# Kernel optimization log

Hardware: AMD Instinct MI355X
Metric: run time of the kernel (lower is better)

## Reference

```python
import jax, jax.numpy as jnp
from jax import lax
import numpy as np

EPS = 1e-5
GROUPS = 32  # conv_dim // 4 = 128 // 4


def setup_inputs() -> dict:
    key = jax.random.key(0)
    ks = jax.random.split(key, 6)
    B, C, H, W = 32, 256, 64, 64
    S = 64            # state_dim
    CD = 2 * S        # conv_dim = 128
    x = jax.random.normal(ks[0], (B, C, H, W), dtype=jnp.float32)
    ln_w = jnp.ones((1, C, 1, 1), dtype=jnp.float32)
    ln_b = jnp.zeros((1, C, 1, 1), dtype=jnp.float32)
    # conv weights, OIHW, fan-in scaled
    w_bcdt = jax.random.normal(ks[1], (CD, C, 1, 1), dtype=jnp.float32) / np.sqrt(C)
    w_gw = jax.random.normal(ks[2], (CD, CD // GROUPS, 3, 3), dtype=jnp.float32) / np.sqrt(9 * CD // GROUPS)
    w_out = jax.random.normal(ks[3], (C, C, 1, 1), dtype=jnp.float32) / np.sqrt(C)
    # A ~ Uniform(1, 16) per original init range
    A = jax.random.uniform(ks[4], (S,), dtype=jnp.float32, minval=1.0, maxval=16.0)
    return {"x": x, "ln_w": ln_w, "ln_b": ln_b, "w_bcdt": w_bcdt, "w_gw": w_gw, "w_out": w_out, "A": A}


def reference(x, ln_w, ln_b, w_bcdt, w_gw, w_out, A):
    B, C, H, W = x.shape
    N = H * W
    # LayerNorm2D over channel dim; torch.var default is unbiased (correction=1)
    mean = jnp.mean(x, axis=1, keepdims=True)
    var = jnp.sum((x - mean) ** 2, axis=1, keepdims=True) / (C - 1)
    xn = (x - mean) / jnp.sqrt(var + EPS) * ln_w + ln_b
    # BCdt_proj: 1x1 conv (no bias, no norm, no act)
    bcdt = jnp.einsum('bchw,oc->bohw', xn, w_bcdt[:, :, 0, 0])
    # gw: 3x3 grouped conv, padding 1
    bcdt = lax.conv_general_dilated(
        bcdt, w_gw, window_strides=(1, 1), padding=[(1, 1), (1, 1)],
        dimension_numbers=('NCHW', 'OIHW', 'NCHW'), feature_group_count=GROUPS)
    # SSD core
    flat = bcdt.reshape(B, -1, N)                       # (B, 2S, N)
    BC, dt = jnp.split(flat, 2, axis=1)                 # each (B, S, N)
    Asm = jax.nn.softmax(dt + A[None, :, None], axis=-1)
    AB = Asm * BC                                       # (B, S, N)
    xf = x.reshape(B, C, N)
    h = jnp.einsum('bcn,bsn->bcs', xf, AB)              # (B, C, S)
    y = jnp.einsum('bcs,bsn->bcn', h, BC)               # (B, C, N)
    y = y.reshape(B, C, H, W)
    # out_proj: 1x1 conv
    y = jnp.einsum('bchw,oc->bohw', y, w_out[:, :, 0, 0])
    return y + x
```

## Files before the change

kernel.cpp:

```cpp
#include <hip/hip_runtime.h>
#include <math.h>

#define BB 32
#define CC 256
#define NPIX 4096
#define SS 64
#define CD 128

typedef __attribute__((ext_vector_type(8))) short bf16x8;
typedef __attribute__((ext_vector_type(4))) float f32x4;
typedef __attribute__((ext_vector_type(8))) unsigned short us8;

#define WS_W1     0u
#define WS_S1     16384u
#define WS_BIAS   16512u
#define WS_WOUTT  16640u
#define WS_BCDT1  82176u
#define WS_AB     82176u
#define WS_BCT    4276480u
#define WS_HPART  8470784u
#define WS_H2OS   10567936u
#define WS_BCDT2  16859392u

__device__ inline short f2bf(float f) {
    union { float f; unsigned u; } v; v.f = f;
    unsigned r = v.u + 0x7fffu + ((v.u >> 16) & 1u);
    return (short)(r >> 16);
}
__device__ inline float bf2f(unsigned short h) {
    union { unsigned u; float f; } v; v.u = ((unsigned)h) << 16;
    return v.f;
}
__device__ inline bf16x8 cvt8(float4 a, float4 b) {
    bf16x8 r;
    r[0]=f2bf(a.x); r[1]=f2bf(a.y); r[2]=f2bf(a.z); r[3]=f2bf(a.w);
    r[4]=f2bf(b.x); r[5]=f2bf(b.y); r[6]=f2bf(b.z); r[7]=f2bf(b.w);
    return r;
}

__global__ __launch_bounds__(256) void k_setup1(const float* __restrict__ w_bcdt,
        const float* __restrict__ ln_w, const float* __restrict__ ln_b,
        unsigned short* __restrict__ W1, float* __restrict__ S1, float* __restrict__ bias) {
    int o = blockIdx.x, c = threadIdx.x;
    float w = w_bcdt[o*256 + c];
    short h = f2bf(w * ln_w[c]);
    W1[o*256 + c] = (unsigned short)h;
    __shared__ float red[256];
    red[c] = bf2f((unsigned short)h);
    __syncthreads();
    for (int off = 128; off > 0; off >>= 1) { if (c < off) red[c] += red[c+off]; __syncthreads(); }
    if (c == 0) S1[o] = red[0];
    __syncthreads();
    red[c] = w * ln_b[c];
    __syncthreads();
    for (int off = 128; off > 0; off >>= 1) { if (c < off) red[c] += red[c+off]; __syncthreads(); }
    if (c == 0) bias[o] = red[0];
}

__global__ __launch_bounds__(256) void k_setup2(const float* __restrict__ w_out,
        float* __restrict__ w_outT) {
    int o = blockIdx.x, c = threadIdx.x;
    w_outT[c*256 + o] = w_out[o*256 + c];
}

__global__ __launch_bounds__(256) void k_proj(const float* __restrict__ x,
        const unsigned short* __restrict__ W1, const float* __restrict__ S1,
        const float* __restrict__ bias, float* __restrict__ bcdt1) {
    int nbase = blockIdx.x * 64;
    int b = blockIdx.y;
    int tt = threadIdx.x;
    int wid = tt >> 6;
    int l = tt & 63;
    int lane16 = l & 15, q = l >> 4;

    __shared__ __align__(16) unsigned short sT[64*264];
    __shared__ float sStat[8][64];
    __shared__ float sM[64], sR[64];

    {
        int n_l = tt & 63;
        int cq = tt >> 6;
        const float* xb = x + (size_t)b*CC*NPIX + nbase + n_l;
        float s = 0.f, sq = 0.f;
        #pragma unroll 8
        for (int i = 0; i < 64; ++i) {
            int c = cq*64 + i;
            float v = xb[(size_t)c*NPIX];
            s += v; sq += v*v;
            sT[n_l*264 + c] = (unsigned short)f2bf(v);
        }
        sStat[cq][n_l] = s; sStat[4+cq][n_l] = sq;
    }
    __syncthreads();
    if (tt < 64) {
        float s  = sStat[0][tt]+sStat[1][tt]+sStat[2][tt]+sStat[3][tt];
        float sq = sStat[4][tt]+sStat[5][tt]+sStat[6][tt]+sStat[7][tt];
        float m = s * (1.0f/256.0f);
        sM[tt] = m;
        sR[tt] = 1.0f / sqrtf((sq - s*m) * (1.0f/255.0f) + 1e-5f);
    }
    __syncthreads();

    f32x4 acc[2][4];
    #pragma unroll
    for (int i = 0; i < 2; ++i)
        #pragma unroll
        for (int j = 0; j < 4; ++j) acc[i][j] = (f32x4){0.f,0.f,0.f,0.f};
    int ob = wid * 32;
    for (int kk = 0; kk < 8; ++kk) {
        int k0 = kk * 32;
        bf16x8 a0 = *(const bf16x8*)(W1 + (size_t)(ob + lane16)*256 + k0 + q*8);
        bf16x8 a1 = *(const bf16x8*)(W1 + (size_t)(ob + 16 + lane16)*256 + k0 + q*8);
        bf16x8 bf[4];
        #pragma unroll
        for (int nt = 0; nt < 4; ++nt)
            bf[nt] = *(const bf16x8*)(sT + (nt*16 + lane16)*264 + k0 + q*8);
        #pragma unroll
        for (int nt = 0; nt < 4; ++nt) {
            acc[0][nt] = __builtin_amdgcn_mfma_f32_16x16x32_bf16(a0, bf[nt], acc[0][nt], 0, 0, 0);
            acc[1][nt] = __builtin_amdgcn_mfma_f32_16x16x32_bf16(a1, bf[nt], acc[1][nt], 0, 0, 0);
        }
    }
    #pragma unroll
    for (int i = 0; i < 2; ++i)
        #pragma unroll
        for (int nt = 0; nt < 4; ++nt) {
            int n_l = nt*16 + lane16;
            float m = sM[n_l], r = sR[n_l];
            #pragma unroll
            for (int rr = 0; rr < 4; ++rr) {
                int o = ob + i*16 + q*4 + rr;
                float g = acc[i][nt][rr];
                float val = r * (g - m * S1[o]) + bias[o];
                bcdt1[((size_t)b*CD + o)*NPIX + nbase + n_l] = val;
            }
        }
}

__global__ __launch_bounds__(256) void k_gconv(const float* __restrict__ bcdt1,
        const float* __restrict__ w_gw, unsigned short* __restrict__ bcdt2) {
    int hbase = blockIdx.x * 16;
    int o = blockIdx.y;
    int b = blockIdx.z;
    int g = o >> 2;
    __shared__ float lin[4*18*66];
    for (int i = threadIdx.x; i < 4*18*66; i += 256) lin[i] = 0.f;
    __syncthreads();
    const float* src = bcdt1 + ((size_t)b*CD + g*4)*NPIX;
    for (int idx = threadIdx.x; idx < 4*18*64; idx += 256) {
        int ch = idx / 1152;
        int rem = idx - ch*1152;
        int rr = rem >> 6;
        int col = rem & 63;
        int grow = hbase - 1 + rr;
        if (grow >= 0 && grow < 64)
            lin[ch*1188 + rr*66 + col + 1] = src[ch*NPIX + grow*64 + col];
    }
    float wreg[36];
    #pragma unroll
    for (int j = 0; j < 36; ++j) wreg[j] = w_gw[o*36 + j];
    __syncthreads();
    int col = threadIdx.x & 63;
    int rsub = threadIdx.x >> 6;
    unsigned short* dst = bcdt2 + ((size_t)b*CD + o)*NPIX;
    #pragma unroll
    for (int qq = 0; qq < 4; ++qq) {
        int rr = rsub + 4*qq;
        float a = 0.f;
        #pragma unroll
        for (int i = 0; i < 4; ++i)
            #pragma unroll
            for (int dh = 0; dh < 3; ++dh)
                #pragma unroll
                for (int dw = 0; dw < 3; ++dw)
                    a = fmaf(wreg[i*9 + dh*3 + dw],
                             lin[i*1188 + (rr+dh)*66 + col + dw], a);
        dst[(hbase+rr)*64 + col] = (unsigned short)f2bf(a);
    }
}

__global__ __launch_bounds__(256) void k_softmax(const unsigned short* __restrict__ bcdt2,
        unsigned short* __restrict__ AB) {
    int s = blockIdx.x, b = blockIdx.y, t = threadIdx.x;
    const us8* dt = (const us8*)(bcdt2 + ((size_t)b*CD + 64 + s)*NPIX);
    const us8* bc = (const us8*)(bcdt2 + ((size_t)b*CD + s)*NPIX);
    us8* ab = (us8*)(AB + ((size_t)b*SS + s)*NPIX);
    float f[16];
    us8 d0 = dt[t], d1 = dt[256 + t];
    #pragma unroll
    for (int j = 0; j < 8; ++j) { f[j] = bf2f(d0[j]); f[8+j] = bf2f(d1[j]); }
    float mx = -1e30f;
    #pragma unroll
    for (int j = 0; j < 16; ++j) mx = fmaxf(mx, f[j]);
    #pragma unroll
    for (int off = 32; off > 0; off >>= 1) mx = fmaxf(mx, __shfl_down(mx, off, 64));
    __shared__ float buf[8];
    int w = t >> 6;
    if ((t & 63) == 0) buf[w] = mx;
    __syncthreads();
    mx = fmaxf(fmaxf(buf[0], buf[1]), fmaxf(buf[2], buf[3]));
    float sum = 0.f;
    #pragma unroll
    for (int j = 0; j < 16; ++j) { f[j] = __expf(f[j] - mx); sum += f[j]; }
    #pragma unroll
    for (int off = 32; off > 0; off >>= 1) sum += __shfl_down(sum, off, 64);
    if ((t & 63) == 0) buf[4+w] = sum;
    __syncthreads();
    float inv = 1.0f / (buf[4] + buf[5] + buf[6] + buf[7]);
    us8 b0 = bc[t], b1 = bc[256 + t];
    us8 o0, o1;
    #pragma unroll
    for (int j = 0; j < 8; ++j) {
        o0[j] = (unsigned short)f2bf(f[j]   * inv * bf2f(b0[j]));
        o1[j] = (unsigned short)f2bf(f[8+j] * inv * bf2f(b1[j]));
    }
    ab[t] = o0; ab[256 + t] = o1;
}

__global__ __launch_bounds__(256) void k_tbc(const unsigned short* __restrict__ bcdt2,
        unsigned short* __restrict__ BCt) {
    int nb = blockIdx.x * 64;
    int b = blockIdx.y;
    __shared__ unsigned short tile[64*65];
    int tt = threadIdx.x;
    #pragma unroll
    for (int k = 0; k < 16; ++k) {
        int idx = k*256 + tt;
        int s = idx >> 6, n = idx & 63;
        tile[s*65 + n] = bcdt2[((size_t)b*CD + s)*NPIX + nb + n];
    }
    __syncthreads();
    #pragma unroll
    for (int k = 0; k < 16; ++k) {
        int idx = k*256 + tt;
        int n = idx >> 6, s = idx & 63;
        BCt[((size_t)b*NPIX + nb + n)*SS + s] = tile[s*65 + n];
    }
}

__global__ __launch_bounds__(256) void k_h(const float* __restrict__ x,
        const unsigned short* __restrict__ AB, float* __restrict__ h_part) {
    int cb = blockIdx.x * 64;
    int kc = blockIdx.y;
    int b = blockIdx.z;
    int tt = threadIdx.x;
    int wid = tt >> 6;
    int l = tt & 63;
    int lane16 = l & 15, q = l >> 4;
    __shared__ __align__(16) float tile[2][64][68];

    f32x4 acc[4][4];
    #pragma unroll
    for (int i = 0; i < 4; ++i)
        #pragma unroll
        for (int j = 0; j < 4; ++j) acc[i][j] = (f32x4){0.f,0.f,0.f,0.f};

    for (int kk = 0; kk < 8; ++kk) {
        int n0 = kc*1024 + wid*256 + kk*32;
        bf16x8 afr[4];
        #pragma unroll
        for (int mt = 0; mt < 4; ++mt) {
            const float* ap = x + ((size_t)b*CC + cb + mt*16 + lane16)*NPIX + n0 + q*8;
            float4 u0 = *(const float4*)ap;
            float4 u1 = *(const float4*)(ap + 4);
            afr[mt] = cvt8(u0, u1);
        }
        bf16x8 bfr[4];
        #pragma unroll
        for (int nt = 0; nt < 4; ++nt)
            bfr[nt] = *(const bf16x8*)(AB + ((size_t)b*SS + nt*16 + lane16)*NPIX + n0 + q*8);
        #pragma unroll
        for (int mt = 0; mt < 4; ++mt)
            #pragma unroll
            for (int nt = 0; nt < 4; ++nt)
                acc[mt][nt] = __builtin_amdgcn_mfma_f32_16x16x32_bf16(afr[mt], bfr[nt], acc[mt][nt], 0, 0, 0);
    }

    if (wid >= 2) {
        #pragma unroll
        for (int mt = 0; mt < 4; ++mt)
            #pragma unroll
            for (int nt = 0; nt < 4; ++nt)
                *(float4*)&tile[wid-2][nt*16 + lane16][mt*16 + q*4] = *(float4*)&acc[mt][nt];
    }
    __syncthreads();
    if (wid < 2) {
        #pragma unroll
        for (int mt = 0; mt < 4; ++mt)
            #pragma unroll
            for (int nt = 0; nt < 4; ++nt) {
                float4 v = *(float4*)&tile[wid][nt*16 + lane16][mt*16 + q*4];
                acc[mt][nt][0] += v.x; acc[mt][nt][1] += v.y;
                acc[mt][nt][2] += v.z; acc[mt][nt][3] += v.w;
            }
    }
    __syncthreads();
    if (wid == 1) {
        #pragma unroll
        for (int mt = 0; mt < 4; ++mt)
            #pragma unroll
            for (int nt = 0; nt < 4; ++nt)
                *(float4*)&tile[0][nt*16 + lane16][mt*16 + q*4] = *(float4*)&acc[mt][nt];
    }
    __syncthreads();
    if (wid == 0) {
        float* dst = h_part + ((size_t)kc*BB + b)*CC*SS;
        #pragma unroll
        for (int mt = 0; mt < 4; ++mt)
            #pragma unroll
            for (int nt = 0; nt < 4; ++nt) {
                float4 v = *(float4*)&tile[0][nt*16 + lane16][mt*16 + q*4];
                int s = nt*16 + lane16;
                #pragma unroll
                for (int rr = 0; rr < 4; ++rr) {
                    int c = cb + mt*16 + q*4 + rr;
                    float pv = acc[mt][nt][rr] + ((const float*)&v)[rr];
                    dst[(size_t)c*SS + s] = pv;
                }
            }
    }
}

__global__ __launch_bounds__(256) void k_h2(const float* __restrict__ h_part,
        const float* __restrict__ w_outT, unsigned short* __restrict__ h2os) {
    int sbase = blockIdx.x * 8;
    int b = blockIdx.y;
    __shared__ float hl[256*8];
    int t = threadIdx.x;
    #pragma unroll
    for (int k = 0; k < 8; ++k) {
        int idx = k*256 + t;
        int c = idx >> 3, sc = idx & 7;
        size_t base = (size_t)b*CC*SS + (size_t)c*SS + sbase + sc;
        hl[idx] = h_part[base]
                + h_part[base + (size_t)1*BB*CC*SS]
                + h_part[base + (size_t)2*BB*CC*SS]
                + h_part[base + (size_t)3*BB*CC*SS];
    }
    __syncthreads();
    float4 a0 = {0,0,0,0}, a1 = {0,0,0,0};
    #pragma unroll 8
    for (int c = 0; c < 256; ++c) {
        float wv = w_outT[c*256 + t];
        float4 h0 = *(const float4*)(hl + c*8);
        float4 h1 = *(const float4*)(hl + c*8 + 4);
        a0.x = fmaf(wv, h0.x, a0.x); a0.y = fmaf(wv, h0.y, a0.y);
        a0.z = fmaf(wv, h0.z, a0.z); a0.w = fmaf(wv, h0.w, a0.w);
        a1.x = fmaf(wv, h1.x, a1.x); a1.y = fmaf(wv, h1.y, a1.y);
        a1.z = fmaf(wv, h1.z, a1.z); a1.w = fmaf(wv, h1.w, a1.w);
    }
    unsigned short* dst = h2os + ((size_t)b*CC + t)*SS + sbase;
    us8 pk;
    pk[0]=(unsigned short)f2bf(a0.x); pk[1]=(unsigned short)f2bf(a0.y);
    pk[2]=(unsigned short)f2bf(a0.z); pk[3]=(unsigned short)f2bf(a0.w);
    pk[4]=(unsigned short)f2bf(a1.x); pk[5]=(unsigned short)f2bf(a1.y);
    pk[6]=(unsigned short)f2bf(a1.z); pk[7]=(unsigned short)f2bf(a1.w);
    *(us8*)dst = pk;
}

__global__ __launch_bounds__(256) void k_out(const float* __restrict__ x,
        const unsigned short* __restrict__ h2os, const unsigned short* __restrict__ BCt,
        float* __restrict__ out) {
    int nb = blockIdx.x * 64;
    int b = blockIdx.y;
    int tt = threadIdx.x;
    int wid = tt >> 6;
    int l = tt & 63;
    int lane16 = l & 15, q = l >> 4;
    int ob = wid * 64;

    f32x4 acc[4][4];
    #pragma unroll
    for (int i = 0; i < 4; ++i)
        #pragma unroll
        for (int j = 0; j < 4; ++j) acc[i][j] = (f32x4){0.f,0.f,0.f,0.f};

    #pragma unroll
    for (int kk = 0; kk < 2; ++kk) {
        int s0 = kk*32;
        bf16x8 afr[4], bfr[4];
        #pragma unroll
        for (int mt = 0; mt < 4; ++mt)
            afr[mt] = *(const bf16x8*)(h2os + ((size_t)b*CC + ob + mt*16 + lane16)*SS + s0 + q*8);
        #pragma unroll
        for (int nt = 0; nt < 4; ++nt)
            bfr[nt] = *(const bf16x8*)(BCt + ((size_t)b*NPIX + nb + nt*16 + lane16)*SS + s0 + q*8);
        #pragma unroll
        for (int mt = 0; mt < 4; ++mt)
            #pragma unroll
            for (int nt = 0; nt < 4; ++nt)
                acc[mt][nt] = __builtin_amdgcn_mfma_f32_16x16x32_bf16(afr[mt], bfr[nt], acc[mt][nt], 0, 0, 0);
    }
    #pragma unroll
    for (int mt = 0; mt < 4; ++mt)
        #pragma unroll
        for (int nt = 0; nt < 4; ++nt) {
            int n = nb + nt*16 + lane16;
            #pragma unroll
            for (int rr = 0; rr < 4; ++rr) {
                int o = ob + mt*16 + q*4 + rr;
                size_t idx = ((size_t)b*CC + o)*NPIX + n;
                out[idx] = acc[mt][nt][rr] + x[idx];
            }
        }
}

extern "C" void kernel_launch(void* const* d_in, const int* in_sizes, int n_in,
                              void* d_out, int out_size, void* d_ws, size_t ws_size,
                              hipStream_t stream) {
    const float* x      = (const float*)d_in[0];
    const float* ln_w   = (const float*)d_in[1];
    const float* ln_b   = (const float*)d_in[2];
    const float* w_bcdt = (const float*)d_in[3];
    const float* w_gw   = (const float*)d_in[4];
    const float* w_out  = (const float*)d_in[5];
    float* ws  = (float*)d_ws;
    float* out = (float*)d_out;

    unsigned short* W1    = (unsigned short*)(ws + WS_W1);
    float* S1             = ws + WS_S1;
    float* bias           = ws + WS_BIAS;
    float* w_outT         = ws + WS_WOUTT;
    float* bcdt1          = ws + WS_BCDT1;
    unsigned short* bcdt2 = (unsigned short*)(ws + WS_BCDT2);
    unsigned short* AB    = (unsigned short*)(ws + WS_AB);
    unsigned short* BCt   = (unsigned short*)(ws + WS_BCT);
    float* h_part         = ws + WS_HPART;
    unsigned short* h2os  = (unsigned short*)(ws + WS_H2OS);

    k_setup1<<<128, 256, 0, stream>>>(w_bcdt, ln_w, ln_b, W1, S1, bias);
    k_setup2<<<256, 256, 0, stream>>>(w_out, w_outT);
    k_proj<<<dim3(64, 32), 256, 0, stream>>>(x, W1, S1, bias, bcdt1);
    k_gconv<<<dim3(4, 128, 32), 256, 0, stream>>>(bcdt1, w_gw, bcdt2);
    k_softmax<<<dim3(64, 32), 256, 0, stream>>>(bcdt2, AB);
    k_tbc<<<dim3(64, 32), 256, 0, stream>>>(bcdt2, BCt);
    k_h<<<dim3(4, 4, 32), 256, 0, stream>>>(x, AB, h_part);
    k_h2<<<dim3(8, 32), 256, 0, stream>>>(h_part, w_outT, h2os);
    k_out<<<dim3(64, 32), 256, 0, stream>>>(x, h2os, BCt, out);
}
```

Baseline: 467.2 us.

## Compute all four group outputs per gconv block and split h reduction eight ways

The grouped 3x3 conv now gives each block a whole group, so it computes all four output channels from one shared-memory tile instead of reloading the same input tile four times. Each thread keeps a 6x3 register window and accumulates a 4x4 block of outputs, and the shared-memory fill no longer zeroes the whole tile first. Separately, the h GEMM's K dimension is split into eight partitions instead of four to double the block count, and k_h2 now sums eight partials. The h_part workspace grows to match, which moves the h2os offset and adds traffic to the partial reduction.

```diff
diff --git a/kernel.cpp b/kernel.cpp
--- a/kernel.cpp
+++ b/kernel.cpp
@@ -19,7 +19,7 @@
 #define WS_AB     82176u
 #define WS_BCT    4276480u
 #define WS_HPART  8470784u
-#define WS_H2OS   10567936u
+#define WS_H2OS   12665088u
 #define WS_BCDT2  16859392u
 
 __device__ inline short f2bf(float f) {
@@ -140,43 +140,61 @@
 __global__ __launch_bounds__(256) void k_gconv(const float* __restrict__ bcdt1,
         const float* __restrict__ w_gw, unsigned short* __restrict__ bcdt2) {
     int hbase = blockIdx.x * 16;
-    int o = blockIdx.y;
+    int g = blockIdx.y;
     int b = blockIdx.z;
-    int g = o >> 2;
-    __shared__ float lin[4*18*66];
-    for (int i = threadIdx.x; i < 4*18*66; i += 256) lin[i] = 0.f;
-    __syncthreads();
-    const float* src = bcdt1 + ((size_t)b*CD + g*4)*NPIX;
-    for (int idx = threadIdx.x; idx < 4*18*64; idx += 256) {
-        int ch = idx / 1152;
-        int rem = idx - ch*1152;
-        int rr = rem >> 6;
-        int col = rem & 63;
-        int grow = hbase - 1 + rr;
-        if (grow >= 0 && grow < 64)
-            lin[ch*1188 + rr*66 + col + 1] = src[ch*NPIX + grow*64 + col];
-    }
-    float wreg[36];
-    #pragma unroll
-    for (int j = 0; j < 36; ++j) wreg[j] = w_gw[o*36 + j];
-    __syncthreads();
-    int col = threadIdx.x & 63;
-    int rsub = threadIdx.x >> 6;
-    unsigned short* dst = bcdt2 + ((size_t)b*CD + o)*NPIX;
-    #pragma unroll
-    for (int qq = 0; qq < 4; ++qq) {
-        int rr = rsub + 4*qq;
-        float a = 0.f;
-        #pragma unroll
-        for (int i = 0; i < 4; ++i)
+    __shared__ float lin[4][18][66];
+    int tt = threadIdx.x;
+    int col = tt & 63, ch = tt >> 6;
+
+    const float* src = bcdt1 + ((size_t)b*CD + g*4 + ch)*NPIX;
+    #pragma unroll
+    for (int k = 0; k < 18; ++k) {
+        int grow = hbase - 1 + k;
+        float v = (grow >= 0 && grow < 64) ? src[grow*64 + col] : 0.f;
+        lin[ch][k][col + 1] = v;
+    }
+    if (col == 0 || col == 63) {
+        int pc = (col == 0) ? 0 : 65;
+        #pragma unroll
+        for (int k = 0; k < 18; ++k) lin[ch][k][pc] = 0.f;
+    }
+    __syncthreads();
+
+    int r0 = ch * 4;
+    float acc[4][4];
+    #pragma unroll
+    for (int oc = 0; oc < 4; ++oc)
+        #pragma unroll
+        for (int r = 0; r < 4; ++r) acc[oc][r] = 0.f;
+
+    #pragma unroll
+    for (int ic = 0; ic < 4; ++ic) {
+        float val[6][3];
+        #pragma unroll
+        for (int rr = 0; rr < 6; ++rr)
+            #pragma unroll
+            for (int dw = 0; dw < 3; ++dw)
+                val[rr][dw] = lin[ic][r0 + rr][col + dw];
+        #pragma unroll
+        for (int oc = 0; oc < 4; ++oc) {
+            const float* wp = w_gw + (size_t)((g*4 + oc)*4 + ic)*9;
             #pragma unroll
             for (int dh = 0; dh < 3; ++dh)
                 #pragma unroll
-                for (int dw = 0; dw < 3; ++dw)
-                    a = fmaf(wreg[i*9 + dh*3 + dw],
-                             lin[i*1188 + (rr+dh)*66 + col + dw], a);
-        dst[(hbase+rr)*64 + col] = (unsigned short)f2bf(a);
-    }
+                for (int dw = 0; dw < 3; ++dw) {
+                    float w = wp[dh*3 + dw];
+                    #pragma unroll
+                    for (int r = 0; r < 4; ++r)
+                        acc[oc][r] = fmaf(w, val[r + dh][dw], acc[oc][r]);
+                }
+        }
+    }
+    unsigned short* dstb = bcdt2 + ((size_t)b*CD + g*4)*NPIX + hbase*64;
+    #pragma unroll
+    for (int oc = 0; oc < 4; ++oc)
+        #pragma unroll
+        for (int r = 0; r < 4; ++r)
+            dstb[(size_t)oc*NPIX + (r0 + r)*64 + col] = (unsigned short)f2bf(acc[oc][r]);
 }
 
 __global__ __launch_bounds__(256) void k_softmax(const unsigned short* __restrict__ bcdt2,
@@ -255,8 +273,9 @@
         #pragma unroll
         for (int j = 0; j < 4; ++j) acc[i][j] = (f32x4){0.f,0.f,0.f,0.f};
 
-    for (int kk = 0; kk < 8; ++kk) {
-        int n0 = kc*1024 + wid*256 + kk*32;
+    #pragma unroll
+    for (int kk = 0; kk < 4; ++kk) {
+        int n0 = kc*512 + wid*128 + kk*32;
         bf16x8 afr[4];
         #pragma unroll
         for (int mt = 0; mt < 4; ++mt) {
@@ -332,10 +351,11 @@
         int idx = k*256 + t;
         int c = idx >> 3, sc = idx & 7;
         size_t base = (size_t)b*CC*SS + (size_t)c*SS + sbase + sc;
-        hl[idx] = h_part[base]
-                + h_part[base + (size_t)1*BB*CC*SS]
-                + h_part[base + (size_t)2*BB*CC*SS]
-                + h_part[base + (size_t)3*BB*CC*SS];
+        float v = 0.f;
+        #pragma unroll
+        for (int p = 0; p < 8; ++p)
+            v += h_part[base + (size_t)p*BB*CC*SS];
+        hl[idx] = v;
     }
     __syncthreads();
     float4 a0 = {0,0,0,0}, a1 = {0,0,0,0};
@@ -431,10 +451,10 @@
     k_setup1<<<128, 256, 0, stream>>>(w_bcdt, ln_w, ln_b, W1, S1, bias);
     k_setup2<<<256, 256, 0, stream>>>(w_out, w_outT);
     k_proj<<<dim3(64, 32), 256, 0, stream>>>(x, W1, S1, bias, bcdt1);
-    k_gconv<<<dim3(4, 128, 32), 256, 0, stream>>>(bcdt1, w_gw, bcdt2);
+    k_gconv<<<dim3(4, 32, 32), 256, 0, stream>>>(bcdt1, w_gw, bcdt2);
     k_softmax<<<dim3(64, 32), 256, 0, stream>>>(bcdt2, AB);
     k_tbc<<<dim3(64, 32), 256, 0, stream>>>(bcdt2, BCt);
-    k_h<<<dim3(4, 4, 32), 256, 0, stream>>>(x, AB, h_part);
+    k_h<<<dim3(4, 8, 32), 256, 0, stream>>>(x, AB, h_part);
     k_h2<<<dim3(8, 32), 256, 0, stream>>>(h_part, w_outT, h2os);
     k_out<<<dim3(64, 32), 256, 0, stream>>>(x, h2os, BCt, out);
 }
```

After: 429.1 us. -8.2%, faster.
